# Optimization experiments

Measured on AMD Instinct MI355X. Metric: run time of the kernel, lower is better.

The kernel has to match this reference:

```python
import jax, jax.numpy as jnp
import numpy as np
from jax import lax

EPS = 1e-12  # F.normalize eps

def _l2norm(x):
    n = jnp.linalg.norm(x, axis=-1, keepdims=True)
    return x / jnp.maximum(n, EPS)

def setup_inputs() -> dict:
    key = jax.random.key(0)
    ks = jax.random.split(key, 8)
    B, C, D, N = 64, 512, 128, 200000
    return {
        "query_input": jax.random.normal(ks[0], (B, C), jnp.float32),
        "keys": jax.random.normal(ks[1], (N, D), jnp.float32),
        "values": jax.random.normal(ks[2], (N, D), jnp.float32),
        "importance": jax.random.uniform(ks[3], (N,), jnp.float32),
        "Wq": jax.random.normal(ks[4], (C, D), jnp.float32) / np.sqrt(C),
        "bq": jnp.zeros((D,), jnp.float32),
        "Wa": jax.random.normal(ks[5], (D,), jnp.float32) / np.sqrt(D),
        "ba": jnp.zeros((1,), jnp.float32),
        "Wc": jax.random.normal(ks[6], (D, D), jnp.float32) / np.sqrt(D),
        "bc": jnp.zeros((D,), jnp.float32),
        "top_k": 8,
    }

def reference(query_input, keys, values, importance, Wq, bq, Wa, ba, Wc, bc, top_k):
    # query projection: [B, D]
    q = query_input @ Wq + bq
    # weighted cosine similarity against all memory keys: [B, N]
    sim = (_l2norm(q) @ _l2norm(keys).T) * importance[None, :]
    # top-k memory indices per batch element: [B, K]
    _, idx = lax.top_k(sim, top_k)
    # gather values: [B, K, D]
    retrieved = values[idx]
    # attention over the K retrieved memories
    logits = retrieved @ Wa + ba[0]          # [B, K]
    scores = jax.nn.softmax(logits, axis=-1)  # [B, K]
    combined = jnp.einsum("bk,bkd->bd", scores, retrieved)
    return combined @ Wc + bc
```

## Files before the change

### kernel.cpp

```cpp
#include <hip/hip_runtime.h>
#include <hip/hip_bf16.h>
#include <math.h>

constexpr int B     = 64;
constexpr int C     = 512;
constexpr int D     = 128;
constexpr int NKEYS = 200000;
constexpr int K     = 8;

constexpr int KT     = 64;
constexpr int NTILES = NKEYS / KT;
constexpr int NBLK2  = 512;
constexpr int KD     = 4;
constexpr int TOPSEL = 48;
constexpr int CAP    = 512;

typedef __attribute__((ext_vector_type(8))) short bf16x8;
typedef __attribute__((ext_vector_type(4))) float f32x4;
typedef unsigned int uint32;

template<int KK>
__device__ __forceinline__ void topk_ins(float (&tv)[KK], int (&ti)[KK], float s, int n) {
    if (s <= tv[KK - 1]) return;
    tv[KK - 1] = s; ti[KK - 1] = n;
#pragma unroll
    for (int j = KK - 1; j > 0; --j) {
        if (tv[j] > tv[j - 1]) {
            float t = tv[j]; tv[j] = tv[j - 1]; tv[j - 1] = t;
            int   u = ti[j]; ti[j] = ti[j - 1]; ti[j - 1] = u;
        }
    }
}

__device__ __forceinline__ short f2bf(float x) {
    __hip_bfloat16 h = __float2bfloat16(x);
    return __builtin_bit_cast(short, h);
}

__device__ __forceinline__ uint32 fkey(float f) {
    uint32 u = __builtin_bit_cast(uint32, f);
    return ((int)u < 0) ? ~u : (u | 0x80000000u);
}

__device__ __forceinline__ void pack_bf4(const float4& f, uint32& lo, uint32& hi) {
    const uint32 a0 = __builtin_bit_cast(uint32, f.x) + 0x8000u;
    const uint32 a1 = __builtin_bit_cast(uint32, f.y) + 0x8000u;
    const uint32 a2 = __builtin_bit_cast(uint32, f.z) + 0x8000u;
    const uint32 a3 = __builtin_bit_cast(uint32, f.w) + 0x8000u;
    lo = __builtin_amdgcn_perm(a1, a0, 0x07060302u);
    hi = __builtin_amdgcn_perm(a3, a2, 0x07060302u);
}

__global__ __launch_bounds__(1024)
void k1_qproj(const float* __restrict__ query, const float* __restrict__ Wq,
              const float* __restrict__ bq, float* __restrict__ qt,
              short* __restrict__ qbfT) {
    const int b = blockIdx.x;
    const int t = threadIdx.x;
    const int d = t & 127;
    const int h = t >> 7;
    const float* qr = query + (size_t)b * C;

    float acc = 0.0f;
    const int c0 = h * (C / 8);
#pragma unroll 8
    for (int c = 0; c < C / 8; ++c)
        acc = fmaf(qr[c0 + c], Wq[(size_t)(c0 + c) * D + d], acc);

    __shared__ float part[8][D];
    part[h][d] = acc;
    __syncthreads();
    if (h == 0) {
        float a = bq[d];
#pragma unroll
        for (int i = 0; i < 8; ++i) a += part[i][d];
        float ss = a * a;
#pragma unroll
        for (int off = 32; off > 0; off >>= 1) ss += __shfl_xor(ss, off);
        __shared__ float w[2];
        if ((d & 63) == 0) w[d >> 6] = ss;
        __syncthreads();
        const float inv = 1.0f / fmaxf(sqrtf(w[0] + w[1]), 1e-12f);
        const float qn = a * inv;
        qt[(size_t)d * B + b] = qn;
        qbfT[(size_t)b * D + d] = f2bf(qn);
    }
}

__global__ __launch_bounds__(512, 2)
void k2_sim_topk(const float* __restrict__ keys, const float* __restrict__ imp,
                 const short* __restrict__ qbfT,
                 float* __restrict__ cval, int* __restrict__ cidx) {
    const int tid  = threadIdx.x;
    const int lane = tid & 63;
    const int w    = __builtin_amdgcn_readfirstlane(tid >> 6);
    const int nb   = w & 3;
    const int wm   = w >> 2;

    __shared__ short klds[2][KT * 128];
    __shared__ float scales[2][KT];
    __shared__ float mvs[2][B][KD];
    __shared__ int   mis[2][B][KD];

    bf16x8 bq[4];
    {
        const int batch  = nb * 16 + (lane & 15);
        const char* qrow = (const char*)(qbfT + (size_t)batch * D);
        const int coff   = (lane >> 4) * 16;
#pragma unroll
        for (int ks = 0; ks < 4; ++ks)
            bq[ks] = *(const bf16x8*)(qrow + ks * 64 + coff);
    }

    float tv[KD]; int ti[KD];
#pragma unroll
    for (int j = 0; j < KD; ++j) { tv[j] = -INFINITY; ti[j] = 0; }

    const int hrow = tid >> 5;
    const int hcol = tid & 31;
    const int wbyte = hrow * 256 + ((hcol * 8) ^ ((hrow & 7) << 4));
    const bool wlane = (hcol < 4);

    auto consume = [&](const float4& f0, const float4& f1, const float4& f2,
                       const float4& f3, float impc, int buf) {
        float s0 = f0.x*f0.x + f0.y*f0.y + f0.z*f0.z + f0.w*f0.w;
        float s1 = f1.x*f1.x + f1.y*f1.y + f1.z*f1.z + f1.w*f1.w;
        float s2 = f2.x*f2.x + f2.y*f2.y + f2.z*f2.z + f2.w*f2.w;
        float s3 = f3.x*f3.x + f3.y*f3.y + f3.z*f3.z + f3.w*f3.w;
        const bool b0 = (lane & 1) != 0, b1 = (lane & 2) != 0;
        float t01 = b0 ? s0 : s1;
        float v01 = (b0 ? s1 : s0) + __shfl_xor(t01, 1);
        float t23 = b0 ? s2 : s3;
        float v23 = (b0 ? s3 : s2) + __shfl_xor(t23, 1);
        float t2 = b1 ? v01 : v23;
        float z  = (b1 ? v23 : v01) + __shfl_xor(t2, 2);
        z += __shfl_xor(z, 4);
        z += __shfl_xor(z, 8);
        z += __shfl_xor(z, 16);

        uint32 pk[8];
        pack_bf4(f0, pk[0], pk[1]);
        pack_bf4(f1, pk[2], pk[3]);
        pack_bf4(f2, pk[4], pk[5]);
        pack_bf4(f3, pk[6], pk[7]);

        char* kb = (char*)klds[buf];
        *(uint2*)(kb + wbyte        ) = make_uint2(pk[0], pk[1]);
        *(uint2*)(kb + wbyte +  4096) = make_uint2(pk[2], pk[3]);
        *(uint2*)(kb + wbyte +  8192) = make_uint2(pk[4], pk[5]);
        *(uint2*)(kb + wbyte + 12288) = make_uint2(pk[6], pk[7]);
        if (wlane)
            scales[buf][(hcol & 3) * 16 + hrow] = impc / fmaxf(sqrtf(z), 1e-12f);
    };

    auto score = [&](int buf, int tile) {
#pragma unroll
        for (int mi = 0; mi < 2; ++mi) {
            const int mk   = wm * 2 + mi;
            const int krow = mk * 16 + (lane & 15);
            const int swk  = (krow & 7) << 4;
            const char* arow = (const char*)klds[buf] + krow * 256;
            const int coff = (lane >> 4) * 16;
            f32x4 acc = {0.f, 0.f, 0.f, 0.f};
#pragma unroll
            for (int ks = 0; ks < 4; ++ks) {
                bf16x8 af = *(const bf16x8*)(arow + ((ks * 64 + coff) ^ swk));
                acc = __builtin_amdgcn_mfma_f32_16x16x32_bf16(af, bq[ks], acc, 0, 0, 0);
            }
            const int kl0 = mk * 16 + (lane >> 4) * 4;
            const f32x4 scv = *(const f32x4*)&scales[buf][kl0];
#pragma unroll
            for (int j = 0; j < 4; ++j)
                topk_ins<KD>(tv, ti, acc[j] * scv[j], tile * KT + kl0 + j);
        }
    };

    int tile = blockIdx.x;
    float4 f0, f1, f2, f3;
    float impc = 0.0f;
    {
        const float4* tb = (const float4*)(keys + (size_t)tile * KT * D);
        f0 = tb[tid]; f1 = tb[512 + tid]; f2 = tb[1024 + tid]; f3 = tb[1536 + tid];
        if (wlane) impc = imp[tile * KT + (hcol & 3) * 16 + hrow];
        consume(f0, f1, f2, f3, impc, 0);
    }
    __syncthreads();

    int cur = 0;
    for (;;) {
        const int nxt = tile + NBLK2;
        const bool has_next = nxt < NTILES;

        if (has_next) {
            const float4* tb = (const float4*)(keys + (size_t)nxt * KT * D);
            f0 = tb[tid]; f1 = tb[512 + tid]; f2 = tb[1024 + tid]; f3 = tb[1536 + tid];
            if (wlane) impc = imp[nxt * KT + (hcol & 3) * 16 + hrow];
        }
        __builtin_amdgcn_sched_barrier(0);

        score(cur, tile);

        if (!has_next) break;

        consume(f0, f1, f2, f3, impc, cur ^ 1);
        __syncthreads();
        tile = nxt;
        cur ^= 1;
    }

#pragma unroll
    for (int off = 16; off <= 32; off <<= 1) {
        float ov[KD]; int oi[KD];
#pragma unroll
        for (int j = 0; j < KD; ++j) { ov[j] = __shfl_xor(tv[j], off); oi[j] = __shfl_xor(ti[j], off); }
#pragma unroll
        for (int j = 0; j < KD; ++j) topk_ins<KD>(tv, ti, ov[j], oi[j]);
    }
    __syncthreads();
    if (lane < 16) {
        const int bb = nb * 16 + lane;
#pragma unroll
        for (int j = 0; j < KD; ++j) { mvs[wm][bb][j] = tv[j]; mis[wm][bb][j] = ti[j]; }
    }
    __syncthreads();

    if (tid < B) {
        const size_t base = ((size_t)tid * NBLK2 + blockIdx.x) * K;
#pragma unroll
        for (int j = 0; j < KD; ++j) {
            cval[base + j]      = mvs[0][tid][j];
            cidx[base + j]      = mis[0][tid][j];
            cval[base + KD + j] = mvs[1][tid][j];
            cidx[base + KD + j] = mis[1][tid][j];
        }
    }
}

__global__ __launch_bounds__(512)
void k34_select_attend(const float* __restrict__ cval, const int* __restrict__ cidx,
                       const float* __restrict__ keys, const float* __restrict__ values,
                       const float* __restrict__ imp, const float* __restrict__ qt,
                       const float* __restrict__ Wa, const float* __restrict__ ba,
                       const float* __restrict__ Wc, const float* __restrict__ bc,
                       float* __restrict__ out) {
    const int b = blockIdx.x;
    const int t = threadIdx.x;
    const int lane = t & 63, w = t >> 6;
    constexpr int NC  = NBLK2 * K;
    constexpr int PER = NC / 512;

    __shared__ uint32 hist[4096];
    __shared__ uint32 coarse[256];
    __shared__ int    candL[CAP];
    __shared__ float  simL[CAP];
    __shared__ float  qs[D];
    __shared__ int    thrBin_s, cnt_s, ncand_s;
    __shared__ int    sel[K];
    __shared__ float  part[2][K];
    __shared__ float  scores[K];
    __shared__ float  comb[D];
    __shared__ float  pc[4][D];

#pragma unroll
    for (int i = 0; i < 8; ++i) hist[t + i * 512] = 0;
    if (t == 0) cnt_s = 0;
    if (t < D) qs[t] = qt[(size_t)t * B + b];
    __syncthreads();

    uint32 oks[PER]; int ids[PER];
    const size_t base = (size_t)b * NC + t;
#pragma unroll
    for (int i = 0; i < PER; ++i) {
        oks[i] = fkey(cval[base + i * 512]);
        ids[i] = cidx[base + i * 512];
    }
#pragma unroll
    for (int i = 0; i < PER; ++i)
        atomicAdd(&hist[oks[i] >> 20], 1u);
    __syncthreads();

    if (t < 256) {
        uint32 cs = 0;
#pragma unroll
        for (int j = 0; j < 16; ++j) cs += hist[t * 16 + j];
        coarse[t] = cs;
    }
    __syncthreads();

    if (t < 64) {
        const uint32 g = coarse[4 * t] + coarse[4 * t + 1]
                       + coarse[4 * t + 2] + coarse[4 * t + 3];
        uint32 suf = g;
#pragma unroll
        for (int off = 1; off < 64; off <<= 1) {
            const uint32 o = __shfl_down(suf, off);
            if (t + off < 64) suf += o;
        }
        const uint32 sufnext = __shfl_down(suf, 1);
        const uint32 above0  = (t == 63) ? 0u : sufnext;
        if (suf >= TOPSEL && (t == 63 || sufnext < TOPSEL)) {
            uint32 above = above0;
            int c = 4 * t + 3;
            while (above + coarse[c] < TOPSEL) { above += coarse[c]; --c; }
            int fb = c * 16 + 15;
            while (above + hist[fb] < TOPSEL) { above += hist[fb]; --fb; }
            thrBin_s = fb;
        }
    }
    __syncthreads();
    const uint32 thrKey = (uint32)thrBin_s << 20;

#pragma unroll
    for (int i = 0; i < PER; ++i) {
        if (oks[i] >= thrKey) {
            const int p = atomicAdd(&cnt_s, 1);
            if (p < CAP) candL[p] = ids[i];
        }
    }
    __syncthreads();
    if (t == 0) ncand_s = min(cnt_s, CAP);
    __syncthreads();
    const int ncand = ncand_s;

    const int sub16 = lane >> 4, l16 = lane & 15;
    for (int r = w * 4 + sub16; r < ncand; r += 32) {
        const int idx = candL[r];
        const float4* kp = (const float4*)(keys + (size_t)idx * D) + l16 * 2;
        const float4 kv0 = kp[0], kv1 = kp[1];
        float dot = kv0.x * qs[8 * l16]     + kv0.y * qs[8 * l16 + 1]
                  + kv0.z * qs[8 * l16 + 2] + kv0.w * qs[8 * l16 + 3]
                  + kv1.x * qs[8 * l16 + 4] + kv1.y * qs[8 * l16 + 5]
                  + kv1.z * qs[8 * l16 + 6] + kv1.w * qs[8 * l16 + 7];
        float ss  = kv0.x*kv0.x + kv0.y*kv0.y + kv0.z*kv0.z + kv0.w*kv0.w
                  + kv1.x*kv1.x + kv1.y*kv1.y + kv1.z*kv1.z + kv1.w*kv1.w;
#pragma unroll
        for (int off = 1; off < 16; off <<= 1) {
            dot += __shfl_xor(dot, off);
            ss  += __shfl_xor(ss, off);
        }
        if (l16 == 0)
            simL[r] = dot * (1.0f / fmaxf(sqrtf(ss), 1e-12f)) * imp[idx];
    }
    __syncthreads();

    if (t < 64) {
        float fv[K]; int fi[K];
#pragma unroll
        for (int j = 0; j < K; ++j) { fv[j] = -INFINITY; fi[j] = 0; }
        for (int r = t; r < ncand; r += 64) topk_ins<K>(fv, fi, simL[r], candL[r]);
#pragma unroll
        for (int off = 1; off <= 32; off <<= 1) {
            float ov[K]; int oi[K];
#pragma unroll
            for (int j = 0; j < K; ++j) { ov[j] = __shfl_xor(fv[j], off); oi[j] = __shfl_xor(fi[j], off); }
#pragma unroll
            for (int j = 0; j < K; ++j) topk_ins<K>(fv, fi, ov[j], oi[j]);
        }
        if (t == 0) {
#pragma unroll
            for (int j = 0; j < K; ++j) sel[j] = fi[j];
        }
    }
    __syncthreads();

    const int d = t & 127;
    float v[K];
#pragma unroll
    for (int k = 0; k < K; ++k) v[k] = values[(size_t)sel[k] * D + d];

    const float wa = Wa[d];
#pragma unroll
    for (int k = 0; k < K; ++k) {
        float p = v[k] * wa;
#pragma unroll
        for (int off = 32; off > 0; off >>= 1) p += __shfl_xor(p, off);
        if (t < 128 && (t & 63) == 0) part[t >> 6][k] = p;
    }
    __syncthreads();
    if (t == 0) {
        float lg[K]; float mx = -INFINITY;
#pragma unroll
        for (int k = 0; k < K; ++k) { lg[k] = part[0][k] + part[1][k] + ba[0]; mx = fmaxf(mx, lg[k]); }
        float sum = 0.0f;
#pragma unroll
        for (int k = 0; k < K; ++k) { lg[k] = expf(lg[k] - mx); sum += lg[k]; }
        const float rs = 1.0f / sum;
#pragma unroll
        for (int k = 0; k < K; ++k) scores[k] = lg[k] * rs;
    }
    __syncthreads();

    if (t < 128) {
        float c = 0.0f;
#pragma unroll
        for (int k = 0; k < K; ++k) c = fmaf(scores[k], v[k], c);
        comb[t] = c;
    }
    __syncthreads();

    {
        const int h = t >> 7;
        float acc = 0.0f;
        const int d0 = h * 32;
#pragma unroll 8
        for (int dd = 0; dd < 32; ++dd)
            acc = fmaf(comb[d0 + dd], Wc[(size_t)(d0 + dd) * D + d], acc);
        pc[h][d] = acc;
    }
    __syncthreads();
    if (t < 128)
        out[(size_t)b * D + t] = bc[t] + pc[0][t] + pc[1][t] + pc[2][t] + pc[3][t];
}

extern "C" void kernel_launch(void* const* d_in, const int* in_sizes, int n_in,
                              void* d_out, int out_size, void* d_ws, size_t ws_size,
                              hipStream_t stream) {
    const float* query = (const float*)d_in[0];
    const float* keys  = (const float*)d_in[1];
    const float* vals  = (const float*)d_in[2];
    const float* imp   = (const float*)d_in[3];
    const float* Wq    = (const float*)d_in[4];
    const float* bq    = (const float*)d_in[5];
    const float* Wa    = (const float*)d_in[6];
    const float* ba    = (const float*)d_in[7];
    const float* Wc    = (const float*)d_in[8];
    const float* bc    = (const float*)d_in[9];

    float* out = (float*)d_out;

    float* qt   = (float*)d_ws;
    short* qbfT = (short*)(qt + (size_t)D * B);
    float* cval = (float*)(qbfT + (size_t)B * D);
    int*   cidx = (int*)(cval + (size_t)B * NBLK2 * K);

    k1_qproj<<<B, 1024, 0, stream>>>(query, Wq, bq, qt, qbfT);
    k2_sim_topk<<<NBLK2, 512, 0, stream>>>(keys, imp, qbfT, cval, cidx);
    k34_select_attend<<<B, 512, 0, stream>>>(cval, cidx, keys, vals, imp, qt,
                                             Wa, ba, Wc, bc, out);
}
```

Measured before the change: 47.96 us.

## Deepen key-tile prefetch to two tiles ahead with ping-pong registers

The main scoring loop now keeps two register sets of key tiles and prefetches the tile two steps ahead, so global loads have a full extra iteration to land before they are converted into LDS. The loop is unrolled by two to alternate between the A and B register sets. In the select kernel, one barrier is removed by having every thread read the candidate count directly after the existing sync. The deeper prefetch doubles the per-thread registers held for staging, which could lower occupancy or cause spills.

```diff
diff --git a/kernel.cpp b/kernel.cpp
--- a/kernel.cpp
+++ b/kernel.cpp
@@ -176,36 +176,54 @@
     };
 
     int tile = blockIdx.x;
-    float4 f0, f1, f2, f3;
-    float impc = 0.0f;
+    int cur  = 0;
+    float4 fA0, fA1, fA2, fA3, fB0, fB1, fB2, fB3;
+    float impA = 0.0f, impB = 0.0f;
     {
-        const float4* tb = (const float4*)(keys + (size_t)tile * KT * D);
-        f0 = tb[tid]; f1 = tb[512 + tid]; f2 = tb[1024 + tid]; f3 = tb[1536 + tid];
-        if (wlane) impc = imp[tile * KT + (hcol & 3) * 16 + hrow];
-        consume(f0, f1, f2, f3, impc, 0);
-    }
-    __syncthreads();
-
-    int cur = 0;
+        const float4* ta = (const float4*)(keys + (size_t)tile * KT * D);
+        fA0 = ta[tid]; fA1 = ta[512 + tid]; fA2 = ta[1024 + tid]; fA3 = ta[1536 + tid];
+        if (wlane) impA = imp[tile * KT + (hcol & 3) * 16 + hrow];
+        const int t1 = tile + NBLK2;
+        if (t1 < NTILES) {
+            const float4* tb = (const float4*)(keys + (size_t)t1 * KT * D);
+            fB0 = tb[tid]; fB1 = tb[512 + tid]; fB2 = tb[1024 + tid]; fB3 = tb[1536 + tid];
+            if (wlane) impB = imp[t1 * KT + (hcol & 3) * 16 + hrow];
+        }
+        consume(fA0, fA1, fA2, fA3, impA, 0);
+    }
+    __syncthreads();
+
     for (;;) {
-        const int nxt = tile + NBLK2;
-        const bool has_next = nxt < NTILES;
-
-        if (has_next) {
-            const float4* tb = (const float4*)(keys + (size_t)nxt * KT * D);
-            f0 = tb[tid]; f1 = tb[512 + tid]; f2 = tb[1024 + tid]; f3 = tb[1536 + tid];
-            if (wlane) impc = imp[nxt * KT + (hcol & 3) * 16 + hrow];
-        }
-        __builtin_amdgcn_sched_barrier(0);
-
-        score(cur, tile);
-
-        if (!has_next) break;
-
-        consume(f0, f1, f2, f3, impc, cur ^ 1);
-        __syncthreads();
-        tile = nxt;
-        cur ^= 1;
+        {
+            const int nxt = tile + NBLK2;
+            if (nxt >= NTILES) { score(cur, tile); break; }
+            const int pre = tile + 2 * NBLK2;
+            if (pre < NTILES) {
+                const float4* tp = (const float4*)(keys + (size_t)pre * KT * D);
+                fA0 = tp[tid]; fA1 = tp[512 + tid]; fA2 = tp[1024 + tid]; fA3 = tp[1536 + tid];
+                if (wlane) impA = imp[pre * KT + (hcol & 3) * 16 + hrow];
+            }
+            __builtin_amdgcn_sched_barrier(0);
+            score(cur, tile);
+            consume(fB0, fB1, fB2, fB3, impB, cur ^ 1);
+            __syncthreads();
+            tile = nxt; cur ^= 1;
+        }
+        {
+            const int nxt = tile + NBLK2;
+            if (nxt >= NTILES) { score(cur, tile); break; }
+            const int pre = tile + 2 * NBLK2;
+            if (pre < NTILES) {
+                const float4* tp = (const float4*)(keys + (size_t)pre * KT * D);
+                fB0 = tp[tid]; fB1 = tp[512 + tid]; fB2 = tp[1024 + tid]; fB3 = tp[1536 + tid];
+                if (wlane) impB = imp[pre * KT + (hcol & 3) * 16 + hrow];
+            }
+            __builtin_amdgcn_sched_barrier(0);
+            score(cur, tile);
+            consume(fA0, fA1, fA2, fA3, impA, cur ^ 1);
+            __syncthreads();
+            tile = nxt; cur ^= 1;
+        }
     }
 
 #pragma unroll
@@ -254,7 +272,7 @@
     __shared__ int    candL[CAP];
     __shared__ float  simL[CAP];
     __shared__ float  qs[D];
-    __shared__ int    thrBin_s, cnt_s, ncand_s;
+    __shared__ int    thrBin_s, cnt_s;
     __shared__ int    sel[K];
     __shared__ float  part[2][K];
     __shared__ float  scores[K];
@@ -318,9 +336,7 @@
         }
     }
     __syncthreads();
-    if (t == 0) ncand_s = min(cnt_s, CAP);
-    __syncthreads();
-    const int ncand = ncand_s;
+    const int ncand = min(cnt_s, CAP);
 
     const int sub16 = lane >> 4, l16 = lane & 15;
     for (int r = w * 4 + sub16; r < ncand; r += 32) {
```

New measurement: 51.59 us. +7.6%, slower.

## Process two key tiles per pipeline stage with fully unrolled fixed schedule

Applied to the files above, without the earlier changes.

The similarity/top-k loop now loads, converts and scores two 64-key tiles per stage instead of one. The LDS buffers are doubled to hold a pair per stage, and the variable-length loop is replaced by a fixed unrolled schedule of three pair-stages plus an optional seventh tile. The aim is more memory loads in flight per wave and half as many block-wide barriers. In exchange it uses twice the LDS and more registers for the second prefetched tile, which could cut occupancy under the 512x2 launch bounds.

```diff
diff --git a/kernel.cpp b/kernel.cpp
--- a/kernel.cpp
+++ b/kernel.cpp
@@ -11,6 +11,7 @@
 constexpr int KT     = 64;
 constexpr int NTILES = NKEYS / KT;
 constexpr int NBLK2  = 512;
+constexpr int EXTRA  = NTILES - 6 * NBLK2;
 constexpr int KD     = 4;
 constexpr int TOPSEL = 48;
 constexpr int CAP    = 512;
@@ -97,8 +98,8 @@
     const int nb   = w & 3;
     const int wm   = w >> 2;
 
-    __shared__ short klds[2][KT * 128];
-    __shared__ float scales[2][KT];
+    __shared__ short klds[2][2][KT * 128];
+    __shared__ float scales[2][2][KT];
     __shared__ float mvs[2][B][KD];
     __shared__ int   mis[2][B][KD];
 
@@ -121,8 +122,15 @@
     const int wbyte = hrow * 256 + ((hcol * 8) ^ ((hrow & 7) << 4));
     const bool wlane = (hcol < 4);
 
+    auto loadt = [&](int tile, float4& f0, float4& f1, float4& f2, float4& f3,
+                     float& impc) {
+        const float4* tb = (const float4*)(keys + (size_t)tile * KT * D);
+        f0 = tb[tid]; f1 = tb[512 + tid]; f2 = tb[1024 + tid]; f3 = tb[1536 + tid];
+        if (wlane) impc = imp[tile * KT + (hcol & 3) * 16 + hrow];
+    };
+
     auto consume = [&](const float4& f0, const float4& f1, const float4& f2,
-                       const float4& f3, float impc, int buf) {
+                       const float4& f3, float impc, int buf, int half) {
         float s0 = f0.x*f0.x + f0.y*f0.y + f0.z*f0.z + f0.w*f0.w;
         float s1 = f1.x*f1.x + f1.y*f1.y + f1.z*f1.z + f1.w*f1.w;
         float s2 = f2.x*f2.x + f2.y*f2.y + f2.z*f2.z + f2.w*f2.w;
@@ -144,22 +152,22 @@
         pack_bf4(f2, pk[4], pk[5]);
         pack_bf4(f3, pk[6], pk[7]);
 
-        char* kb = (char*)klds[buf];
+        char* kb = (char*)klds[buf][half];
         *(uint2*)(kb + wbyte        ) = make_uint2(pk[0], pk[1]);
         *(uint2*)(kb + wbyte +  4096) = make_uint2(pk[2], pk[3]);
         *(uint2*)(kb + wbyte +  8192) = make_uint2(pk[4], pk[5]);
         *(uint2*)(kb + wbyte + 12288) = make_uint2(pk[6], pk[7]);
         if (wlane)
-            scales[buf][(hcol & 3) * 16 + hrow] = impc / fmaxf(sqrtf(z), 1e-12f);
+            scales[buf][half][(hcol & 3) * 16 + hrow] = impc / fmaxf(sqrtf(z), 1e-12f);
     };
 
-    auto score = [&](int buf, int tile) {
+    auto score = [&](int buf, int half, int tile) {
 #pragma unroll
         for (int mi = 0; mi < 2; ++mi) {
             const int mk   = wm * 2 + mi;
             const int krow = mk * 16 + (lane & 15);
             const int swk  = (krow & 7) << 4;
-            const char* arow = (const char*)klds[buf] + krow * 256;
+            const char* arow = (const char*)klds[buf][half] + krow * 256;
             const int coff = (lane >> 4) * 16;
             f32x4 acc = {0.f, 0.f, 0.f, 0.f};
 #pragma unroll
@@ -168,44 +176,59 @@
                 acc = __builtin_amdgcn_mfma_f32_16x16x32_bf16(af, bq[ks], acc, 0, 0, 0);
             }
             const int kl0 = mk * 16 + (lane >> 4) * 4;
-            const f32x4 scv = *(const f32x4*)&scales[buf][kl0];
+            const f32x4 scv = *(const f32x4*)&scales[buf][half][kl0];
 #pragma unroll
             for (int j = 0; j < 4; ++j)
                 topk_ins<KD>(tv, ti, acc[j] * scv[j], tile * KT + kl0 + j);
         }
     };
 
-    int tile = blockIdx.x;
-    float4 f0, f1, f2, f3;
-    float impc = 0.0f;
+    const int bid  = blockIdx.x;
+    const bool has7 = bid < EXTRA;
+
+    float4 fA0, fA1, fA2, fA3, fB0, fB1, fB2, fB3;
+    float impA = 0.0f, impB = 0.0f;
+
+    loadt(bid,          fA0, fA1, fA2, fA3, impA);
+    loadt(bid + NBLK2,  fB0, fB1, fB2, fB3, impB);
+    consume(fA0, fA1, fA2, fA3, impA, 0, 0);
+    consume(fB0, fB1, fB2, fB3, impB, 0, 1);
+    __syncthreads();
+
+    int cur = 0;
+#pragma unroll
+    for (int p = 0; p < 2; ++p) {
+        const int tA = bid + (2 * p) * NBLK2;
+        const int tB = tA + NBLK2;
+        const int nA = bid + (2 * p + 2) * NBLK2;
+        const int nB = nA + NBLK2;
+        loadt(nA, fA0, fA1, fA2, fA3, impA);
+        loadt(nB, fB0, fB1, fB2, fB3, impB);
+        __builtin_amdgcn_sched_barrier(0);
+        score(cur, 0, tA);
+        score(cur, 1, tB);
+        consume(fA0, fA1, fA2, fA3, impA, cur ^ 1, 0);
+        consume(fB0, fB1, fB2, fB3, impB, cur ^ 1, 1);
+        __syncthreads();
+        cur ^= 1;
+    }
+
     {
-        const float4* tb = (const float4*)(keys + (size_t)tile * KT * D);
-        f0 = tb[tid]; f1 = tb[512 + tid]; f2 = tb[1024 + tid]; f3 = tb[1536 + tid];
-        if (wlane) impc = imp[tile * KT + (hcol & 3) * 16 + hrow];
-        consume(f0, f1, f2, f3, impc, 0);
-    }
-    __syncthreads();
-
-    int cur = 0;
-    for (;;) {
-        const int nxt = tile + NBLK2;
-        const bool has_next = nxt < NTILES;
-
-        if (has_next) {
-            const float4* tb = (const float4*)(keys + (size_t)nxt * KT * D);
-            f0 = tb[tid]; f1 = tb[512 + tid]; f2 = tb[1024 + tid]; f3 = tb[1536 + tid];
-            if (wlane) impc = imp[nxt * KT + (hcol & 3) * 16 + hrow];
-        }
-        __builtin_amdgcn_sched_barrier(0);
-
-        score(cur, tile);
-
-        if (!has_next) break;
-
-        consume(f0, f1, f2, f3, impc, cur ^ 1);
-        __syncthreads();
-        tile = nxt;
-        cur ^= 1;
+        const int tA = bid + 4 * NBLK2;
+        const int tB = tA + NBLK2;
+        if (has7) {
+            const int t6 = bid + 6 * NBLK2;
+            loadt(t6, fA0, fA1, fA2, fA3, impA);
+            __builtin_amdgcn_sched_barrier(0);
+            score(cur, 0, tA);
+            score(cur, 1, tB);
+            consume(fA0, fA1, fA2, fA3, impA, cur ^ 1, 0);
+            __syncthreads();
+            score(cur ^ 1, 0, t6);
+        } else {
+            score(cur, 0, tA);
+            score(cur, 1, tB);
+        }
     }
 
 #pragma unroll
```

Result: slower. 51.02 us (+6.4%).
